# Performance work log

Measured on AMD Instinct MI355X. Metric: run time of the kernel, lower is better.

## Reference

```python
import jax, jax.numpy as jnp
import numpy as np

EPS = 1e-12


def hedgehog_feature_map(W, x):
    # W: [H, D, F], x: [B, H, L, D] -> [B, H, L, 2F]
    o = jnp.einsum('hdf,bhld->bhlf', W, x)
    phi = jnp.concatenate([jax.nn.softmax(o, axis=-1), jax.nn.softmax(-o, axis=-1)], axis=-1)
    return jnp.clip(phi, EPS, None)


def setup_inputs() -> dict:
    key = jax.random.key(0)
    k1, k2, k3, k4, k5 = jax.random.split(key, 5)
    B, H, L, D = 2, 16, 2048, 64
    NFM, F = 4, 64
    q = jax.random.normal(k1, (B, H, L, D), dtype=jnp.float32)
    k = jax.random.normal(k2, (B, H, L, D), dtype=jnp.float32)
    v = jax.random.normal(k3, (B, H, L, D), dtype=jnp.float32)
    # kaiming-uniform-like init for the feature-map projections
    bound = np.sqrt(6.0 / D)
    Wq = jax.random.uniform(k4, (NFM, H, D, F), minval=-bound, maxval=bound, dtype=jnp.float32)
    Wk = jax.random.uniform(k5, (NFM, H, D, F), minval=-bound, maxval=bound, dtype=jnp.float32)
    return {"q": q, "k": k, "v": v, "Wq": Wq, "Wk": Wk, "layer_idx": 0}


def reference(q, k, v, Wq, Wk, layer_idx):
    phi_q = hedgehog_feature_map(Wq[layer_idx], q)  # [B,H,L,2F]
    phi_k = hedgehog_feature_map(Wk[layer_idx], k)  # [B,H,L,2F]
    a = jnp.einsum('bhmf,bhnf->bhmn', phi_q, phi_k)  # [B,H,L,L]
    L = a.shape[-1]
    causal = jnp.tril(jnp.ones((L, L), dtype=bool))  # keep lower-triangular incl. diag
    a = jnp.where(causal, a, 0.0)
    a = a / (jnp.sum(a, axis=-1, keepdims=True) + EPS)
    return jnp.einsum('bhmn,bhnd->bhmd', a, v)
```

## Files before the change

kernel.cpp:

```cpp
#include <hip/hip_runtime.h>

#define BH_N   32
#define H_N    16
#define L_N    2048
#define D_N    64
#define F_N    64
#define FF_N   128
#define CH_N   64
#define NC_N   32
#define EPSF   1e-12f

#define S_STRIDE (D_N*FF_N)
#define S_TOTAL  ((size_t)BH_N*NC_N*S_STRIDE)
#define Z_TOTAL  ((size_t)BH_N*NC_N*FF_N)
#define WT_HEAD  (F_N*D_N)
#define WT_MAT   (H_N*WT_HEAD)

typedef unsigned short u16;
typedef short bf16x8 __attribute__((ext_vector_type(8)));
typedef float f32x4  __attribute__((ext_vector_type(4)));

#define MFMA16(A,B,C) __builtin_amdgcn_mfma_f32_16x16x32_bf16(A,B,C,0,0,0)

__device__ __forceinline__ void split_hl(float x, u16& h, u16& l){
  unsigned u = __float_as_uint(x);
  h = (u16)(u >> 16);
  float hf = __uint_as_float(u & 0xffff0000u);
  l = (u16)(__float_as_uint(x - hf) >> 16);
}

__device__ __forceinline__ int ix128(int r, int c){ return (r*128 + c) ^ ((r&7)<<3); }
__device__ __forceinline__ int ix64 (int r, int c){ return (r*64  + c) ^ ((r&7)<<3); }
__device__ __forceinline__ int ixA  (int r, int c){ return (r*64  + c) ^ ((r&7)<<2); }

__device__ __forceinline__ bf16x8 ldf128(const u16* t, int r, int k0){
  return *reinterpret_cast<const bf16x8*>(t + ix128(r,k0));
}
__device__ __forceinline__ bf16x8 ldf64(const u16* t, int r, int k0){
  return *reinterpret_cast<const bf16x8*>(t + ix64(r,k0));
}

__device__ __forceinline__ void cvt8(const float* __restrict__ p, bf16x8& h8, bf16x8& l8){
  f32x4 a = *reinterpret_cast<const f32x4*>(p);
  f32x4 b = *reinterpret_cast<const f32x4*>(p+4);
  float v[8] = {a[0],a[1],a[2],a[3],b[0],b[1],b[2],b[3]};
  #pragma unroll
  for (int i=0;i<8;++i){ u16 hh,ll; split_hl(v[i],hh,ll); h8[i]=(short)hh; l8[i]=(short)ll; }
}

__device__ __forceinline__ void o_mfma(const float* __restrict__ X,
                                       const u16* __restrict__ WTh,
                                       const u16* __restrict__ WTl,
                                       int m0, int lane, f32x4 oacc[4])
{
  int lrow = lane&15, k0l = (lane>>4)*8;
  bf16x8 xh[2], xl[2];
  #pragma unroll
  for (int ks=0; ks<2; ++ks)
    cvt8(X + (size_t)(m0+lrow)*D_N + ks*32 + k0l, xh[ks], xl[ks]);
  #pragma unroll
  for (int ft=0; ft<4; ++ft) oacc[ft] = (f32x4){0.f,0.f,0.f,0.f};
  #pragma unroll
  for (int ks=0; ks<2; ++ks){
    #pragma unroll
    for (int ft=0; ft<4; ++ft){
      const u16* bp = WTh + (ft*16+lrow)*D_N + ks*32 + k0l;
      const u16* bq = WTl + (ft*16+lrow)*D_N + ks*32 + k0l;
      bf16x8 wh = *reinterpret_cast<const bf16x8*>(bp);
      bf16x8 wl = *reinterpret_cast<const bf16x8*>(bq);
      oacc[ft] = MFMA16(xh[ks], wh, oacc[ft]);
      oacc[ft] = MFMA16(xh[ks], wl, oacc[ft]);
      oacc[ft] = MFMA16(xl[ks], wh, oacc[ft]);
    }
  }
}

__device__ __forceinline__ void softmax_cl(const f32x4 oacc[4], f32x4 pP[4], f32x4 pM[4])
{
  #pragma unroll
  for (int reg=0; reg<4; ++reg){
    float mP = fmaxf(fmaxf(oacc[0][reg],oacc[1][reg]), fmaxf(oacc[2][reg],oacc[3][reg]));
    float mM = fminf(fminf(oacc[0][reg],oacc[1][reg]), fminf(oacc[2][reg],oacc[3][reg]));
    #pragma unroll
    for (int o=8;o>0;o>>=1){ mP = fmaxf(mP,__shfl_xor(mP,o,64)); mM = fminf(mM,__shfl_xor(mM,o,64)); }
    float eP[4], eM[4], sP=0.f, sM=0.f;
    #pragma unroll
    for (int ft=0; ft<4; ++ft){
      eP[ft] = __expf(oacc[ft][reg]-mP);
      eM[ft] = __expf(mM-oacc[ft][reg]);
      sP += eP[ft]; sM += eM[ft];
    }
    #pragma unroll
    for (int o=8;o>0;o>>=1){ sP += __shfl_xor(sP,o,64); sM += __shfl_xor(sM,o,64); }
    float iP = 1.f/sP, iM = 1.f/sM;
    #pragma unroll
    for (int ft=0; ft<4; ++ft){
      pP[ft][reg] = fmaxf(eP[ft]*iP, EPSF);
      pM[ft][reg] = fmaxf(eM[ft]*iM, EPSF);
    }
  }
}

__device__ __forceinline__ void store_phi_rm(u16* th, u16* tl, int m0, int lane,
                                             const f32x4 pP[4], const f32x4 pM[4]){
  int lrow = lane&15, lkg = lane>>4;
  #pragma unroll
  for (int reg=0; reg<4; ++reg){
    int m = m0 + lkg*4 + reg;
    #pragma unroll
    for (int ft=0; ft<4; ++ft){
      int f = ft*16 + lrow;
      u16 hh,ll;
      split_hl(pP[ft][reg],hh,ll); th[ix128(m,f)]    = hh; tl[ix128(m,f)]    = ll;
      split_hl(pM[ft][reg],hh,ll); th[ix128(m,64+f)] = hh; tl[ix128(m,64+f)] = ll;
    }
  }
}

__device__ __forceinline__ void store_phi_tr(u16* th, u16* tl, int m0, int lane,
                                             const f32x4 pP[4], const f32x4 pM[4]){
  int lrow = lane&15, lkg = lane>>4;
  #pragma unroll
  for (int reg=0; reg<4; ++reg){
    int m = m0 + lkg*4 + reg;
    #pragma unroll
    for (int ft=0; ft<4; ++ft){
      int f = ft*16 + lrow;
      u16 hh,ll;
      split_hl(pP[ft][reg],hh,ll); th[ix64(f,m)]    = hh; tl[ix64(f,m)]    = ll;
      split_hl(pM[ft][reg],hh,ll); th[ix64(64+f,m)] = hh; tl[ix64(64+f,m)] = ll;
    }
  }
}

__global__ __launch_bounds__(256)
void hh_wprep(const float* __restrict__ Wq, const float* __restrict__ Wk,
              const int* __restrict__ lidx, u16* __restrict__ WT)
{
  __shared__ float tile[64*65];
  int bid = blockIdx.x, which = bid & 1, h = bid >> 1;
  const float* Wsrc = (which ? Wk : Wq) + (size_t)(*lidx)*(H_N*D_N*F_N) + (size_t)h*(D_N*F_N);
  u16* dh = WT + which*(2*WT_MAT) + h*WT_HEAD;
  u16* dl = dh + WT_MAT;
  int t = threadIdx.x;
  #pragma unroll
  for (int i=0;i<16;++i){
    int idx = i*256 + t;
    tile[(idx&63)*65 + (idx>>6)] = Wsrc[idx];
  }
  __syncthreads();
  #pragma unroll
  for (int i=0;i<16;++i){
    int idx = i*256 + t;
    float w = tile[(idx>>6)*65 + (idx&63)];
    u16 hh,ll; split_hl(w,hh,ll);
    dh[idx] = hh; dl[idx] = ll;
  }
}

__global__ __launch_bounds__(256,3)
void hh_chunksums(const float* __restrict__ kin, const float* __restrict__ vin,
                  const u16* __restrict__ WkT,
                  float* __restrict__ S_ws, float* __restrict__ z_ws)
{
  __shared__ __align__(16) char sm[51200];
  u16*  pkT_h = (u16*)sm;
  u16*  pkT_l = (u16*)(sm + 16384);
  u16*  vt_h  = (u16*)(sm + 32768);
  u16*  vt_l  = (u16*)(sm + 40960);
  float* zb   = (float*)(sm + 49152);

  int bid = blockIdx.x, bh = bid>>5, c = bid & (NC_N-1), h = bh & (H_N-1);
  const float* Xk = kin + ((size_t)bh*L_N + c*CH_N)*D_N;
  const float* Vc = vin + ((size_t)bh*L_N + c*CH_N)*D_N;
  const u16* Wh = WkT + h*WT_HEAD;
  const u16* Wl = Wh + WT_MAT;
  int t = threadIdx.x, lane = t&63, w = t>>6;

  int vn = t>>2, vd0 = (t&3)*16;
  float4 vreg[4];
  #pragma unroll
  for (int p=0;p<4;++p)
    vreg[p] = *reinterpret_cast<const float4*>(Vc + (size_t)vn*D_N + vd0 + p*4);

  f32x4 oacc[4], pP[4], pM[4];
  o_mfma(Xk, Wh, Wl, w*16, lane, oacc);
  softmax_cl(oacc, pP, pM);
  store_phi_tr(pkT_h, pkT_l, w*16, lane, pP, pM);

  #pragma unroll
  for (int ft=0; ft<4; ++ft){
    float sP = pP[ft][0]+pP[ft][1]+pP[ft][2]+pP[ft][3];
    float sM = pM[ft][0]+pM[ft][1]+pM[ft][2]+pM[ft][3];
    sP += __shfl_xor(sP,16,64); sP += __shfl_xor(sP,32,64);
    sM += __shfl_xor(sM,16,64); sM += __shfl_xor(sM,32,64);
    if ((lane>>4)==0){
      zb[w*128 + ft*16 + lane]      = sP;
      zb[w*128 + 64 + ft*16 + lane] = sM;
    }
  }

  #pragma unroll
  for (int p=0;p<4;++p){
    float vals[4] = {vreg[p].x, vreg[p].y, vreg[p].z, vreg[p].w};
    #pragma unroll
    for (int e=0;e<4;++e){
      int d = vd0 + p*4 + e;
      u16 hh,ll; split_hl(vals[e],hh,ll);
      vt_h[ix64(d, vn)] = hh;
      vt_l[ix64(d, vn)] = ll;
    }
  }
  __syncthreads();

  if (t < FF_N)
    z_ws[(size_t)(bh*NC_N + c)*FF_N + t] = zb[t] + zb[128+t] + zb[256+t] + zb[384+t];

  int m0 = w*16, lrow = lane&15, k0l = (lane>>4)*8;
  f32x4 acc[8];
  #pragma unroll
  for (int ft=0; ft<8; ++ft) acc[ft] = (f32x4){0.f,0.f,0.f,0.f};
  #pragma unroll
  for (int ks=0; ks<2; ++ks){
    int r0k = ks*32 + k0l;
    bf16x8 ah = ldf64(vt_h, m0 + lrow, r0k);
    bf16x8 al = ldf64(vt_l, m0 + lrow, r0k);
    #pragma unroll
    for (int ft=0; ft<8; ++ft){
      bf16x8 bh = ldf64(pkT_h, ft*16 + lrow, r0k);
      bf16x8 bl = ldf64(pkT_l, ft*16 + lrow, r0k);
      acc[ft] = MFMA16(ah, bh, acc[ft]);
      acc[ft] = MFMA16(ah, bl, acc[ft]);
      acc[ft] = MFMA16(al, bh, acc[ft]);
    }
  }
  float* Sout = S_ws + (size_t)(bh*NC_N + c)*S_STRIDE;
  #pragma unroll
  for (int ft=0; ft<8; ++ft)
    #pragma unroll
    for (int reg=0; reg<4; ++reg){
      int d = m0 + (lane>>4)*4 + reg;
      Sout[(size_t)d*FF_N + ft*16 + lrow] = acc[ft][reg];
    }
}

__global__ __launch_bounds__(256)
void hh_scan(float* __restrict__ S_ws, float* __restrict__ z_ws)
{
  int bid = blockIdx.x;
  int bh = bid / 33, s = bid % 33;
  int t = threadIdx.x;
  if (s < 32){
    size_t base = (size_t)bh*NC_N*S_STRIDE + (size_t)s*256 + t;
    float run = 0.f;
    float nxt = S_ws[base];
    #pragma unroll
    for (int c=0;c<NC_N;++c){
      float cur = nxt;
      if (c+1 < NC_N) nxt = S_ws[base + (size_t)(c+1)*S_STRIDE];
      S_ws[base + (size_t)c*S_STRIDE] = run;
      run += cur;
    }
  } else if (t < FF_N){
    size_t base = (size_t)bh*NC_N*FF_N + t;
    float run = 0.f;
    float nxt = z_ws[base];
    #pragma unroll
    for (int c=0;c<NC_N;++c){
      float cur = nxt;
      if (c+1 < NC_N) nxt = z_ws[base + (size_t)(c+1)*FF_N];
      z_ws[base + (size_t)c*FF_N] = run;
      run += cur;
    }
  }
}

__global__ __launch_bounds__(256,3)
void hh_output(const float* __restrict__ qin, const float* __restrict__ kin,
               const float* __restrict__ vin,
               const u16* __restrict__ WT,
               const float* __restrict__ S_ws, const float* __restrict__ z_ws,
               float* __restrict__ out)
{
  __shared__ __align__(16) char sm[32768];
  u16*  ph   = (u16*)sm;
  u16*  pl   = (u16*)(sm + 16384);
  float* aA  = (float*)sm;
  u16*  vt_h = (u16*)(sm + 16384);
  u16*  vt_l = (u16*)(sm + 24576);

  int bid = blockIdx.x, bh = bid>>5, c = bid & (NC_N-1), h = bh & (H_N-1);
  const float* Xq = qin + ((size_t)bh*L_N + c*CH_N)*D_N;
  const float* Xk = kin + ((size_t)bh*L_N + c*CH_N)*D_N;
  const float* Vc = vin + ((size_t)bh*L_N + c*CH_N)*D_N;
  const float* Sp = S_ws + (size_t)(bh*NC_N + c)*S_STRIDE;
  const float* zp = z_ws + (size_t)(bh*NC_N + c)*FF_N;
  const u16* WqTh = WT + h*WT_HEAD;
  const u16* WqTl = WqTh + WT_MAT;
  const u16* WkTh = WT + 2*WT_MAT + h*WT_HEAD;
  const u16* WkTl = WkTh + WT_MAT;
  int t = threadIdx.x, lane = t&63, w = t>>6;
  int m0 = w*16, lrow = lane&15, lkg = lane>>4, k0l = lkg*8;

  f32x4 oacc[4], pP[4], pM[4];
  o_mfma(Xq, WqTh, WqTl, m0, lane, oacc);
  softmax_cl(oacc, pP, pM);

  float dz[4];
  {
    float zqP[4], zqM[4];
    #pragma unroll
    for (int ft=0; ft<4; ++ft){
      zqP[ft] = zp[ft*16 + lrow];
      zqM[ft] = zp[64 + ft*16 + lrow];
    }
    #pragma unroll
    for (int reg=0; reg<4; ++reg){
      float s = 0.f;
      #pragma unroll
      for (int ft=0; ft<4; ++ft)
        s += pP[ft][reg]*zqP[ft] + pM[ft][reg]*zqM[ft];
      #pragma unroll
      for (int o=8;o>0;o>>=1) s += __shfl_xor(s,o,64);
      dz[reg] = s;
    }
  }

  store_phi_rm(ph, pl, m0, lane, pP, pM);
  bf16x8 qh[4], ql[4];
  #pragma unroll
  for (int ks=0; ks<4; ++ks){
    qh[ks] = ldf128(ph, m0 + lrow, ks*32 + k0l);
    ql[ks] = ldf128(pl, m0 + lrow, ks*32 + k0l);
  }

  o_mfma(Xk, WkTh, WkTl, m0, lane, oacc);
  softmax_cl(oacc, pP, pM);
  store_phi_rm(ph, pl, m0, lane, pP, pM);

  int vn = t>>2, vd0 = (t&3)*16;
  float4 vreg[4];
  #pragma unroll
  for (int p=0;p<4;++p)
    vreg[p] = *reinterpret_cast<const float4*>(Vc + (size_t)vn*D_N + vd0 + p*4);

  __syncthreads();

  f32x4 accA[4], accO[4];
  #pragma unroll
  for (int i=0;i<4;++i){ accA[i]=(f32x4){0,0,0,0}; accO[i]=(f32x4){0,0,0,0}; }

  #pragma unroll
  for (int ks=0; ks<4; ++ks){
    int f0 = ks*32 + k0l;
    #pragma unroll
    for (int nt=0; nt<4; ++nt){
      if (nt <= w){
        bf16x8 kh = ldf128(ph, nt*16 + lrow, f0);
        bf16x8 kl = ldf128(pl, nt*16 + lrow, f0);
        accA[nt] = MFMA16(qh[ks], kh, accA[nt]);
        accA[nt] = MFMA16(qh[ks], kl, accA[nt]);
        accA[nt] = MFMA16(ql[ks], kh, accA[nt]);
      }
    }
    #pragma unroll
    for (int dt=0; dt<4; ++dt){
      bf16x8 sh, sl;
      cvt8(Sp + (size_t)(dt*16 + lrow)*FF_N + f0, sh, sl);
      accO[dt] = MFMA16(qh[ks], sh, accO[dt]);
      accO[dt] = MFMA16(qh[ks], sl, accO[dt]);
      accO[dt] = MFMA16(ql[ks], sh, accO[dt]);
    }
  }

  float rs[4] = {0.f,0.f,0.f,0.f};
  #pragma unroll
  for (int nt=0; nt<4; ++nt)
    #pragma unroll
    for (int reg=0; reg<4; ++reg){
      float a = accA[nt][reg];
      if (nt > w) a = 0.f;
      if (nt == w && lrow > lkg*4 + reg) a = 0.f;
      accA[nt][reg] = a;
      rs[reg] += a;
    }
  float den[4];
  #pragma unroll
  for (int reg=0; reg<4; ++reg){
    float s = rs[reg];
    s += __shfl_xor(s,1,64); s += __shfl_xor(s,2,64);
    s += __shfl_xor(s,4,64); s += __shfl_xor(s,8,64);
    den[reg] = dz[reg] + s + EPSF;
  }

  __syncthreads();

  #pragma unroll
  for (int nt=0; nt<4; ++nt)
    #pragma unroll
    for (int reg=0; reg<4; ++reg){
      int m = m0 + lkg*4 + reg;
      aA[ixA(m, nt*16 + lrow)] = accA[nt][reg];
    }
  #pragma unroll
  for (int p=0;p<4;++p){
    float vals[4] = {vreg[p].x, vreg[p].y, vreg[p].z, vreg[p].w};
    #pragma unroll
    for (int e=0;e<4;++e){
      int d = vd0 + p*4 + e;
      u16 hh,ll; split_hl(vals[e],hh,ll);
      vt_h[ix64(d, vn)] = hh;
      vt_l[ix64(d, vn)] = ll;
    }
  }
  __syncthreads();

  #pragma unroll
  for (int ks=0; ks<2; ++ks){
    if (ks <= (w>>1)){
      int n0 = ks*32 + k0l;
      int m  = m0 + lrow;
      f32x4 a0 = *reinterpret_cast<const f32x4*>(aA + ixA(m, n0));
      f32x4 a1 = *reinterpret_cast<const f32x4*>(aA + ixA(m, n0+4));
      float av[8] = {a0[0],a0[1],a0[2],a0[3],a1[0],a1[1],a1[2],a1[3]};
      bf16x8 Ah, Al;
      #pragma unroll
      for (int i=0;i<8;++i){ u16 hh,ll; split_hl(av[i],hh,ll); Ah[i]=(short)hh; Al[i]=(short)ll; }
      #pragma unroll
      for (int dt=0; dt<4; ++dt){
        bf16x8 vh = ldf64(vt_h, dt*16 + lrow, n0);
        bf16x8 vl = ldf64(vt_l, dt*16 + lrow, n0);
        accO[dt] = MFMA16(Ah, vh, accO[dt]);
        accO[dt] = MFMA16(Ah, vl, accO[dt]);
        accO[dt] = MFMA16(Al, vh, accO[dt]);
      }
    }
  }

  #pragma unroll
  for (int reg=0; reg<4; ++reg){
    float inv = 1.0f / den[reg];
    int m = m0 + lkg*4 + reg;
    float* orow = out + ((size_t)bh*L_N + c*CH_N + m)*D_N;
    #pragma unroll
    for (int dt=0; dt<4; ++dt)
      orow[dt*16 + lrow] = accO[dt][reg] * inv;
  }
}

extern "C" void kernel_launch(void* const* d_in, const int* in_sizes, int n_in,
                              void* d_out, int out_size, void* d_ws, size_t ws_size,
                              hipStream_t stream) {
  const float* q    = (const float*)d_in[0];
  const float* k    = (const float*)d_in[1];
  const float* v    = (const float*)d_in[2];
  const float* Wq   = (const float*)d_in[3];
  const float* Wk   = (const float*)d_in[4];
  const int*   lidx = (const int*)d_in[5];
  float* out  = (float*)d_out;
  float* S_ws = (float*)d_ws;
  float* z_ws = S_ws + S_TOTAL;
  u16*   WT   = (u16*)((char*)d_ws + (S_TOTAL + Z_TOTAL)*sizeof(float));

  hh_wprep    <<<2*H_N,     256, 0, stream>>>(Wq, Wk, lidx, WT);
  hh_chunksums<<<BH_N*NC_N, 256, 0, stream>>>(k, v, WT + 2*WT_MAT, S_ws, z_ws);
  hh_scan     <<<BH_N*33,   256, 0, stream>>>(S_ws, z_ws);
  hh_output   <<<BH_N*NC_N, 256, 0, stream>>>(q, k, v, WT, S_ws, z_ws, out);
}
```

Baseline: 169.5 us.

## Store chunk state as split bf16 hi/lo pairs and hoist state MFMA earlier

The chunk-sum kernel now writes the per-chunk state S as separate bf16 high and low halves instead of fp32. The scan kernel is reworked to read and write these pairs two elements at a time, and the output kernel loads them directly as MFMA operands, so the fp32-to-bf16 split no longer runs in the hot loop. The S·phi_q MFMA loop is also moved ahead of the key feature-map computation, which may help overlap global loads with compute. Workspace traffic stays the same size, and the scan re-splits running sums, which adds a small rounding difference.

```diff
diff --git a/kernel.cpp b/kernel.cpp
--- a/kernel.cpp
+++ b/kernel.cpp
@@ -11,12 +11,13 @@
 #define EPSF   1e-12f
 
 #define S_STRIDE (D_N*FF_N)
-#define S_TOTAL  ((size_t)BH_N*NC_N*S_STRIDE)
+#define SH_TOTAL ((size_t)BH_N*NC_N*S_STRIDE)
 #define Z_TOTAL  ((size_t)BH_N*NC_N*FF_N)
 #define WT_HEAD  (F_N*D_N)
 #define WT_MAT   (H_N*WT_HEAD)
 
 typedef unsigned short u16;
+typedef unsigned int   u32;
 typedef short bf16x8 __attribute__((ext_vector_type(8)));
 typedef float f32x4  __attribute__((ext_vector_type(4)));
 
@@ -161,7 +162,8 @@
 __global__ __launch_bounds__(256,3)
 void hh_chunksums(const float* __restrict__ kin, const float* __restrict__ vin,
                   const u16* __restrict__ WkT,
-                  float* __restrict__ S_ws, float* __restrict__ z_ws)
+                  u16* __restrict__ Sh_ws, u16* __restrict__ Sl_ws,
+                  float* __restrict__ z_ws)
 {
   __shared__ __align__(16) char sm[51200];
   u16*  pkT_h = (u16*)sm;
@@ -234,32 +236,43 @@
       acc[ft] = MFMA16(al, bh, acc[ft]);
     }
   }
-  float* Sout = S_ws + (size_t)(bh*NC_N + c)*S_STRIDE;
+  u16* Shout = Sh_ws + (size_t)(bh*NC_N + c)*S_STRIDE;
+  u16* Slout = Sl_ws + (size_t)(bh*NC_N + c)*S_STRIDE;
   #pragma unroll
   for (int ft=0; ft<8; ++ft)
     #pragma unroll
     for (int reg=0; reg<4; ++reg){
       int d = m0 + (lane>>4)*4 + reg;
-      Sout[(size_t)d*FF_N + ft*16 + lrow] = acc[ft][reg];
+      int idx = d*FF_N + ft*16 + lrow;
+      u16 hh,ll; split_hl(acc[ft][reg],hh,ll);
+      Shout[idx] = hh; Slout[idx] = ll;
     }
 }
 
 __global__ __launch_bounds__(256)
-void hh_scan(float* __restrict__ S_ws, float* __restrict__ z_ws)
+void hh_scan(u16* __restrict__ Sh_ws, u16* __restrict__ Sl_ws,
+             float* __restrict__ z_ws)
 {
   int bid = blockIdx.x;
-  int bh = bid / 33, s = bid % 33;
+  int bh = bid / 17, s = bid % 17;
   int t = threadIdx.x;
-  if (s < 32){
-    size_t base = (size_t)bh*NC_N*S_STRIDE + (size_t)s*256 + t;
-    float run = 0.f;
-    float nxt = S_ws[base];
-    #pragma unroll
-    for (int c=0;c<NC_N;++c){
-      float cur = nxt;
-      if (c+1 < NC_N) nxt = S_ws[base + (size_t)(c+1)*S_STRIDE];
-      S_ws[base + (size_t)c*S_STRIDE] = run;
-      run += cur;
+  if (s < 16){
+    size_t base = (size_t)bh*NC_N*S_STRIDE + (size_t)s*512 + 2*t;
+    float run0 = 0.f, run1 = 0.f;
+    u32 nh = *reinterpret_cast<const u32*>(Sh_ws + base);
+    u32 nl = *reinterpret_cast<const u32*>(Sl_ws + base);
+    #pragma unroll
+    for (int c=0; c<NC_N; ++c){
+      u32 ch = nh, cl = nl;
+      if (c+1 < NC_N){
+        nh = *reinterpret_cast<const u32*>(Sh_ws + base + (size_t)(c+1)*S_STRIDE);
+        nl = *reinterpret_cast<const u32*>(Sl_ws + base + (size_t)(c+1)*S_STRIDE);
+      }
+      u16 h0,l0,h1,l1; split_hl(run0,h0,l0); split_hl(run1,h1,l1);
+      *reinterpret_cast<u32*>(Sh_ws + base + (size_t)c*S_STRIDE) = (u32)h0 | ((u32)h1<<16);
+      *reinterpret_cast<u32*>(Sl_ws + base + (size_t)c*S_STRIDE) = (u32)l0 | ((u32)l1<<16);
+      run0 += __uint_as_float((ch & 0xffffu) << 16) + __uint_as_float((cl & 0xffffu) << 16);
+      run1 += __uint_as_float(ch & 0xffff0000u)     + __uint_as_float(cl & 0xffff0000u);
     }
   } else if (t < FF_N){
     size_t base = (size_t)bh*NC_N*FF_N + t;
@@ -279,7 +292,8 @@
 void hh_output(const float* __restrict__ qin, const float* __restrict__ kin,
                const float* __restrict__ vin,
                const u16* __restrict__ WT,
-               const float* __restrict__ S_ws, const float* __restrict__ z_ws,
+               const u16* __restrict__ Sh_ws, const u16* __restrict__ Sl_ws,
+               const float* __restrict__ z_ws,
                float* __restrict__ out)
 {
   __shared__ __align__(16) char sm[32768];
@@ -293,7 +307,8 @@
   const float* Xq = qin + ((size_t)bh*L_N + c*CH_N)*D_N;
   const float* Xk = kin + ((size_t)bh*L_N + c*CH_N)*D_N;
   const float* Vc = vin + ((size_t)bh*L_N + c*CH_N)*D_N;
-  const float* Sp = S_ws + (size_t)(bh*NC_N + c)*S_STRIDE;
+  const u16* Sph = Sh_ws + (size_t)(bh*NC_N + c)*S_STRIDE;
+  const u16* Spl = Sl_ws + (size_t)(bh*NC_N + c)*S_STRIDE;
   const float* zp = z_ws + (size_t)(bh*NC_N + c)*FF_N;
   const u16* WqTh = WT + h*WT_HEAD;
   const u16* WqTl = WqTh + WT_MAT;
@@ -334,6 +349,22 @@
     ql[ks] = ldf128(pl, m0 + lrow, ks*32 + k0l);
   }
 
+  f32x4 accA[4], accO[4];
+  #pragma unroll
+  for (int i=0;i<4;++i){ accA[i]=(f32x4){0,0,0,0}; accO[i]=(f32x4){0,0,0,0}; }
+  #pragma unroll
+  for (int ks=0; ks<4; ++ks){
+    int f0 = ks*32 + k0l;
+    #pragma unroll
+    for (int dt=0; dt<4; ++dt){
+      bf16x8 sh = *reinterpret_cast<const bf16x8*>(Sph + (size_t)(dt*16 + lrow)*FF_N + f0);
+      bf16x8 sl = *reinterpret_cast<const bf16x8*>(Spl + (size_t)(dt*16 + lrow)*FF_N + f0);
+      accO[dt] = MFMA16(qh[ks], sh, accO[dt]);
+      accO[dt] = MFMA16(qh[ks], sl, accO[dt]);
+      accO[dt] = MFMA16(ql[ks], sh, accO[dt]);
+    }
+  }
+
   o_mfma(Xk, WkTh, WkTl, m0, lane, oacc);
   softmax_cl(oacc, pP, pM);
   store_phi_rm(ph, pl, m0, lane, pP, pM);
@@ -345,10 +376,6 @@
     vreg[p] = *reinterpret_cast<const float4*>(Vc + (size_t)vn*D_N + vd0 + p*4);
 
   __syncthreads();
-
-  f32x4 accA[4], accO[4];
-  #pragma unroll
-  for (int i=0;i<4;++i){ accA[i]=(f32x4){0,0,0,0}; accO[i]=(f32x4){0,0,0,0}; }
 
   #pragma unroll
   for (int ks=0; ks<4; ++ks){
@@ -362,14 +389,6 @@
         accA[nt] = MFMA16(qh[ks], kl, accA[nt]);
         accA[nt] = MFMA16(ql[ks], kh, accA[nt]);
       }
-    }
-    #pragma unroll
-    for (int dt=0; dt<4; ++dt){
-      bf16x8 sh, sl;
-      cvt8(Sp + (size_t)(dt*16 + lrow)*FF_N + f0, sh, sl);
-      accO[dt] = MFMA16(qh[ks], sh, accO[dt]);
-      accO[dt] = MFMA16(qh[ks], sl, accO[dt]);
-      accO[dt] = MFMA16(ql[ks], sh, accO[dt]);
     }
   }
 
@@ -458,12 +477,13 @@
   const float* Wk   = (const float*)d_in[4];
   const int*   lidx = (const int*)d_in[5];
   float* out  = (float*)d_out;
-  float* S_ws = (float*)d_ws;
-  float* z_ws = S_ws + S_TOTAL;
-  u16*   WT   = (u16*)((char*)d_ws + (S_TOTAL + Z_TOTAL)*sizeof(float));
+  u16*   Sh_ws = (u16*)d_ws;
+  u16*   Sl_ws = Sh_ws + SH_TOTAL;
+  float* z_ws  = (float*)(Sl_ws + SH_TOTAL);
+  u16*   WT    = (u16*)(z_ws + Z_TOTAL);
 
   hh_wprep    <<<2*H_N,     256, 0, stream>>>(Wq, Wk, lidx, WT);
-  hh_chunksums<<<BH_N*NC_N, 256, 0, stream>>>(k, v, WT + 2*WT_MAT, S_ws, z_ws);
-  hh_scan     <<<BH_N*33,   256, 0, stream>>>(S_ws, z_ws);
-  hh_output   <<<BH_N*NC_N, 256, 0, stream>>>(q, k, v, WT, S_ws, z_ws, out);
-}
+  hh_chunksums<<<BH_N*NC_N, 256, 0, stream>>>(k, v, WT + 2*WT_MAT, Sh_ws, Sl_ws, z_ws);
+  hh_scan     <<<BH_N*17,   256, 0, stream>>>(Sh_ws, Sl_ws, z_ws);
+  hh_output   <<<BH_N*NC_N, 256, 0, stream>>>(q, k, v, WT, Sh_ws, Sl_ws, z_ws, out);
+}
```

After: 187.4 us. 1.11x slower.
